# Performance work log

Measured on AMD Instinct MI355X. Metric: run time of the kernel, lower is better.

## Reference

```python
import jax, jax.numpy as jnp
import numpy as np

N_HEADS = 16
D_IN = 1024
D_K = 64          # per-head
D_V_HEAD = 1024 // N_HEADS  # 64 per-head


def setup_inputs() -> dict:
    key = jax.random.key(0)
    k1, k2, k3, k4, k5 = jax.random.split(key, 5)
    B, LQ, LK = 2, 2048, 2048
    s = 1.0 / np.sqrt(D_IN)
    return {
        "input_q": jax.random.normal(k1, (B, LQ, D_IN), dtype=jnp.float32),
        "input_k": jax.random.normal(k2, (B, LK, D_IN), dtype=jnp.float32),
        # nn.Linear weights stored as [out, in]; we use [in, out] for x @ W
        "wq": jax.random.uniform(k3, (D_IN, D_K * N_HEADS), jnp.float32, -s, s),
        "wk": jax.random.uniform(k4, (D_IN, D_K * N_HEADS), jnp.float32, -s, s),
        "wv": jax.random.uniform(k5, (D_IN, D_V_HEAD * N_HEADS), jnp.float32, -s, s),
    }


def reference(input_q, input_k, wq, wk, wv):
    B, LQ, _ = input_q.shape
    _, LK, _ = input_k.shape
    # project and split heads: [B, H, L, d]
    q = (input_q @ wq).reshape(B, LQ, N_HEADS, D_K).transpose(0, 2, 1, 3)
    k = (input_k @ wk).reshape(B, LK, N_HEADS, D_K).transpose(0, 2, 1, 3)
    v = (input_k @ wv).reshape(B, LK, N_HEADS, D_V_HEAD).transpose(0, 2, 1, 3)
    attn = jnp.einsum("bhqd,bhkd->bhqk", q, k) / jnp.sqrt(jnp.float32(D_K))
    attn = jax.nn.softmax(attn, axis=-1)
    out = jnp.einsum("bhqk,bhkd->bhqd", attn, v)
    return out.transpose(0, 2, 1, 3).reshape(B, LQ, D_V_HEAD * N_HEADS)
```

## Files before the change

kernel.cpp:

```cpp
#include <hip/hip_runtime.h>

#define DIN 1024
#define LSEQ 2048

typedef _Float16 f16;
typedef _Float16 half8 __attribute__((ext_vector_type(8)));
typedef float floatx4 __attribute__((ext_vector_type(4)));

__device__ __forceinline__ void async_ld16(const void* g, void* l) {
  __builtin_amdgcn_global_load_lds(
      (const __attribute__((address_space(1))) void*)g,
      (__attribute__((address_space(3))) void*)l, 16, 0, 0);
}

__device__ __forceinline__ float fast_exp2(float x) {
#if __has_builtin(__builtin_amdgcn_exp2f)
  return __builtin_amdgcn_exp2f(x);
#else
  return exp2f(x);
#endif
}

__device__ __forceinline__ unsigned int pack2_f16(float a, float b) {
#if __has_builtin(__builtin_amdgcn_cvt_pkrtz)
  typedef __fp16 fp16x2 __attribute__((ext_vector_type(2)));
  fp16x2 h = __builtin_amdgcn_cvt_pkrtz(a, b);
  return __builtin_bit_cast(unsigned int, h);
#else
  union { f16 h[2]; unsigned int u; } pk;
  pk.h[0] = (f16)a; pk.h[1] = (f16)b;
  return pk.u;
#endif
}

__global__ void __launch_bounds__(256) kprep(const float* __restrict__ xq,
                                             const float* __restrict__ xk,
                                             const float* __restrict__ wq,
                                             const float* __restrict__ wk,
                                             const float* __restrict__ wv,
                                             f16* __restrict__ wqt,
                                             f16* __restrict__ wkt,
                                             f16* __restrict__ wvt,
                                             f16* __restrict__ xqh,
                                             f16* __restrict__ xkh) {
  int z = blockIdx.z;
  int tid = threadIdx.x;
  if (z < 3) {
    __shared__ float t[32][33];
    const float* src = z == 0 ? wq : (z == 1 ? wk : wv);
    f16* dst = z == 0 ? wqt : (z == 1 ? wkt : wvt);
    int k0 = blockIdx.x * 32, n0 = blockIdx.y * 32;
    int tx = tid & 31, ty = tid >> 5;
#pragma unroll
    for (int r = 0; r < 4; ++r)
      t[ty + r * 8][tx] = src[(k0 + ty + r * 8) * DIN + n0 + tx];
    __syncthreads();
#pragma unroll
    for (int r = 0; r < 4; ++r)
      dst[(n0 + ty + r * 8) * DIN + k0 + tx] = (f16)t[tx][ty + r * 8];
  } else {
    const float4* src = (const float4*)(z == 4 ? xk : xq);
    uint2* dst = (uint2*)(z == 4 ? xkh : xqh);
    int bx = blockIdx.y * 32 + blockIdx.x;
    int i = bx * 256 + tid;
#pragma unroll
    for (int it = 0; it < 4; ++it, i += 262144) {
      float4 v = src[i];
      union { unsigned int u[2]; uint2 w; } pk;
      pk.u[0] = pack2_f16(v.x, v.y);
      pk.u[1] = pack2_f16(v.z, v.w);
      dst[i] = pk.w;
    }
  }
}

template <int AMODE>
__global__ void __launch_bounds__(256) kproj(const float* __restrict__ xq,
                                             const float* __restrict__ xk,
                                             const f16* __restrict__ xqh,
                                             const f16* __restrict__ xkh,
                                             const f16* __restrict__ wqt,
                                             const f16* __restrict__ wkt,
                                             const f16* __restrict__ wvt,
                                             f16* __restrict__ qb,
                                             f16* __restrict__ kb,
                                             f16* __restrict__ vtb) {
  __shared__ __align__(16) char smem[34816];
  char* As = smem;
  char* Bs = smem + 16384;
  const float* X;
  const f16* Xh;
  const f16* W;
  int z = blockIdx.z;
  if (z == 0) { X = xq; Xh = xqh; W = wqt; }
  else if (z == 1) { X = xk; Xh = xkh; W = wkt; }
  else { X = xk; Xh = xkh; W = wvt; }
  float oscale = (z == 0) ? 0.18033688011112042f : 1.0f;
  int m0 = blockIdx.y * 128, n0 = blockIdx.x * 128;
  int tid = threadIdx.x, lane = tid & 63, wid = tid >> 6;
  int wm = wid >> 1, wn = wid & 1;
  int c15 = lane & 15, g = lane >> 4;
  int l8 = lane >> 3, l7 = lane & 7;
  int kk = 8 * (l7 ^ l8);
  int swz = (c15 & 7) << 4;
  floatx4 acc[4][4] = {};

  for (int kt = 0; kt < 16; ++kt) {
    int k0 = kt * 64;
    if constexpr (AMODE == 1) {
#pragma unroll
      for (int cc = 0; cc < 4; ++cc) {
        int c = wid * 4 + cc;
        async_ld16(&Xh[(m0 + c * 8 + l8) * DIN + k0 + kk], As + c * 1024);
        async_ld16(&W[(n0 + c * 8 + l8) * DIN + k0 + kk], Bs + c * 1024);
      }
    } else {
#pragma unroll
      for (int cc = 0; cc < 4; ++cc) {
        int c = wid * 4 + cc;
        async_ld16(&W[(n0 + c * 8 + l8) * DIN + k0 + kk], Bs + c * 1024);
      }
      int q = tid & 15;
#pragma unroll
      for (int p = 0; p < 8; ++p) {
        int row = p * 16 + (tid >> 4);
        const float4 v = *(const float4*)&X[(m0 + row) * DIN + k0 + q * 4];
        union { unsigned int u[2]; uint2 v2; } pk;
        pk.u[0] = pack2_f16(v.x, v.y);
        pk.u[1] = pack2_f16(v.z, v.w);
        *(uint2*)(As + row * 128 + ((q * 8) ^ ((row & 7) << 4))) = pk.v2;
      }
    }
    __syncthreads();
#pragma unroll
    for (int ks = 0; ks < 2; ++ks) {
      int koff = (ks * 64 + g * 16) ^ swz;
      half8 af[4], bf[4];
#pragma unroll
      for (int i = 0; i < 4; ++i)
        af[i] = *(const half8*)(As + (wm * 64 + i * 16 + c15) * 128 + koff);
#pragma unroll
      for (int j = 0; j < 4; ++j)
        bf[j] = *(const half8*)(Bs + (wn * 64 + j * 16 + c15) * 128 + koff);
#pragma unroll
      for (int i = 0; i < 4; ++i)
#pragma unroll
        for (int j = 0; j < 4; ++j)
          acc[i][j] = __builtin_amdgcn_mfma_f32_16x16x32_f16(af[i], bf[j], acc[i][j], 0, 0, 0);
    }
    __syncthreads();
  }

  if (z != 2) {
    f16* dst = (z == 0) ? qb : kb;
#pragma unroll
    for (int i = 0; i < 4; ++i) {
      int mrow = m0 + wm * 64 + i * 16 + 4 * g;
#pragma unroll
      for (int j = 0; j < 4; ++j) {
        int n = n0 + wn * 64 + j * 16 + c15;
        int h = n >> 6, d = n & 63;
#pragma unroll
        for (int r = 0; r < 4; ++r) {
          int m = mrow + r;
          int b = m >> 11, lrow = m & 2047;
          dst[(((b << 4) + h) * 2048 + lrow) * 64 + d] = (f16)(acc[i][j][r] * oscale);
        }
      }
    }
  } else {
#pragma unroll
    for (int i = 0; i < 4; ++i) {
      int mb = (wm * 64 + i * 16 + 4 * g) * 2;
#pragma unroll
      for (int j = 0; j < 4; ++j) {
        int nl = wn * 64 + j * 16 + c15;
        union { unsigned int u[2]; uint2 v; } pk;
        pk.u[0] = pack2_f16(acc[i][j][0], acc[i][j][1]);
        pk.u[1] = pack2_f16(acc[i][j][2], acc[i][j][3]);
        *(uint2*)(smem + nl * 272 + mb) = pk.v;
      }
    }
    __syncthreads();
    int rowp = tid >> 1, halfp = tid & 1;
    int n = n0 + rowp, h = n >> 6, d = n & 63;
    int b = m0 >> 11, lbase = m0 & 2047;
    f16* dstp = vtb + (((size_t)b * 16 + h) * 64 + d) * 2048 + lbase + halfp * 64;
    const char* srcl = smem + rowp * 272 + halfp * 128;
#pragma unroll
    for (int u = 0; u < 8; ++u)
      *(uint4*)(dstp + u * 8) = *(const uint4*)(srcl + u * 16);
  }
}

__global__ void __launch_bounds__(256, 2) kattn(const f16* __restrict__ qb,
                                                const f16* __restrict__ kbuf,
                                                const f16* __restrict__ vt,
                                                float* __restrict__ out) {
  __shared__ __align__(16) char smem[81920];
  char* Qs = smem + 65536;
  float* Ot = (float*)smem;
  float* lsb = (float*)(smem + 34816);

  int id = blockIdx.x;
  int wi = id >> 3;
  int bh = ((id & 7) << 2) | (wi >> 4);
  int q0 = (wi & 15) << 7;

  int tid = threadIdx.x, lane = tid & 63, w = tid >> 6;
  int c15 = lane & 15, g = lane >> 4;
  int l8 = lane >> 3, l7 = lane & 7;
  int kk = 8 * (l7 ^ l8);
  int swz = (c15 & 7) << 4;

  const f16* kbase = kbuf + (size_t)bh * 2048 * 64;
  const f16* vbase = vt + (size_t)bh * 64 * 2048;

  auto stageK = [&](int b, int kv0) {
#pragma unroll
    for (int cc = 0; cc < 4; ++cc) {
      int c = w * 4 + cc;
      async_ld16(&kbase[(kv0 + c * 8 + l8) * 64 + kk],
                 smem + b * 16384 + c * 1024);
    }
  };
  auto stageV = [&](int b, int kv0) {
#pragma unroll
    for (int cc = 0; cc < 4; ++cc) {
      int c = w * 4 + cc;
      int hb = c >> 3;
      int dv = (c & 7) * 8 + l8;
      async_ld16(&vbase[(size_t)dv * 2048 + kv0 + 64 * hb + kk],
                 smem + 32768 + b * 16384 + c * 1024);
    }
  };

#pragma unroll
  for (int cc = 0; cc < 4; ++cc) {
    int c = w * 4 + cc;
    async_ld16(&qb[((size_t)bh * 2048 + q0 + c * 8 + l8) * 64 + kk],
               Qs + c * 1024);
  }
  stageK(0, 0);
  stageV(0, 0);
  __syncthreads();
  half8 qf[2][2];
#pragma unroll
  for (int s = 0; s < 2; ++s)
#pragma unroll
    for (int ks = 0; ks < 2; ++ks)
      qf[s][ks] = *(const half8*)(Qs + (w * 32 + s * 16 + c15) * 128 +
                                  ((ks * 64 + g * 16) ^ swz));
  __syncthreads();

  float ls0 = 0.f, ls1 = 0.f;
  floatx4 oacc[2][4] = {};
  char* Pw0 = smem + 65536 + (w * 2 + 0) * 2048 + c15 * 128;
  char* Pw1 = smem + 65536 + (w * 2 + 1) * 2048 + c15 * 128;
  int psw = swz;

  for (int t = 0; t < 16; ++t) {
    int buf = t & 1;
    if (t < 15) {
      stageK(buf ^ 1, (t + 1) * 128);
      stageV(buf ^ 1, (t + 1) * 128);
    }

    floatx4 st[2][8] = {};
    __builtin_amdgcn_s_setprio(1);
#pragma unroll
    for (int hb = 0; hb < 2; ++hb) {
      const char* Ks = smem + buf * 16384 + hb * 8192;
#pragma unroll
      for (int ks = 0; ks < 2; ++ks) {
        int koff = (ks * 64 + g * 16) ^ swz;
#pragma unroll
        for (int i = 0; i < 4; ++i) {
          half8 kf = *(const half8*)(Ks + (i * 16 + c15) * 128 + koff);
          st[0][hb * 4 + i] = __builtin_amdgcn_mfma_f32_16x16x32_f16(
              kf, qf[0][ks], st[0][hb * 4 + i], 0, 0, 0);
          st[1][hb * 4 + i] = __builtin_amdgcn_mfma_f32_16x16x32_f16(
              kf, qf[1][ks], st[1][hb * 4 + i], 0, 0, 0);
        }
      }
    }
    __builtin_amdgcn_s_setprio(0);

    unsigned int pu0[16], pu1[16];
    {
      float ps0 = 0.f, ps1 = 0.f;
#pragma unroll
      for (int x = 0; x < 16; ++x) {
        float p0 = fast_exp2(st[0][x >> 1][(x & 1) * 2]);
        float p1 = fast_exp2(st[0][x >> 1][(x & 1) * 2 + 1]);
        ps0 += p0;
        ps1 += p1;
        pu0[x] = pack2_f16(p0, p1);
      }
      ls0 += ps0 + ps1;
    }
    {
      float ps0 = 0.f, ps1 = 0.f;
#pragma unroll
      for (int x = 0; x < 16; ++x) {
        float p0 = fast_exp2(st[1][x >> 1][(x & 1) * 2]);
        float p1 = fast_exp2(st[1][x >> 1][(x & 1) * 2 + 1]);
        ps0 += p0;
        ps1 += p1;
        pu1[x] = pack2_f16(p0, p1);
      }
      ls1 += ps0 + ps1;
    }

    __builtin_amdgcn_s_setprio(1);
#pragma unroll
    for (int hb = 0; hb < 2; ++hb) {
#pragma unroll
      for (int ii = 0; ii < 4; ++ii) {
        union { unsigned int u[2]; uint2 v; } pk;
        pk.u[0] = pu0[hb * 8 + 2 * ii];
        pk.u[1] = pu0[hb * 8 + 2 * ii + 1];
        *(uint2*)(Pw0 + ((32 * ii + 8 * g) ^ psw)) = pk.v;
        pk.u[0] = pu1[hb * 8 + 2 * ii];
        pk.u[1] = pu1[hb * 8 + 2 * ii + 1];
        *(uint2*)(Pw1 + ((32 * ii + 8 * g) ^ psw)) = pk.v;
      }
      const char* Vs = smem + 32768 + buf * 16384 + hb * 8192;
#pragma unroll
      for (int kb = 0; kb < 2; ++kb) {
        half8 pf0 = *(const half8*)(Pw0 + ((kb * 64 + 16 * g) ^ psw));
        half8 pf1 = *(const half8*)(Pw1 + ((kb * 64 + 16 * g) ^ psw));
        int koff = (kb * 64 + g * 16) ^ swz;
#pragma unroll
        for (int df = 0; df < 4; ++df) {
          half8 vf = *(const half8*)(Vs + (df * 16 + c15) * 128 + koff);
          oacc[0][df] = __builtin_amdgcn_mfma_f32_16x16x32_f16(vf, pf0, oacc[0][df], 0, 0, 0);
          oacc[1][df] = __builtin_amdgcn_mfma_f32_16x16x32_f16(vf, pf1, oacc[1][df], 0, 0, 0);
        }
      }
    }
    __builtin_amdgcn_s_setprio(0);
    __syncthreads();
  }

  ls0 += __shfl_xor(ls0, 16, 64);
  ls0 += __shfl_xor(ls0, 32, 64);
  ls1 += __shfl_xor(ls1, 16, 64);
  ls1 += __shfl_xor(ls1, 32, 64);
  if (g == 0) {
    lsb[w * 32 + c15] = ls0;
    lsb[w * 32 + 16 + c15] = ls1;
  }

#pragma unroll
  for (int s = 0; s < 2; ++s)
#pragma unroll
    for (int df = 0; df < 4; ++df)
      *(floatx4*)&Ot[(w * 32 + s * 16 + c15) * 68 + df * 16 + 4 * g] =
          oacc[s][df];
  __syncthreads();

  int b = bh >> 4, h = bh & 15;
  int row = tid >> 1, seg = tid & 1;
  float inv = 1.f / lsb[row];
  float* dstp = &out[((size_t)b * 2048 + q0 + row) * 1024 + h * 64 + seg * 32];
  const float* srcl = &Ot[row * 68 + seg * 32];
#pragma unroll
  for (int u = 0; u < 8; ++u) {
    floatx4 v = *(const floatx4*)(srcl + u * 4) * inv;
    *(floatx4*)(dstp + u * 4) = v;
  }
}

extern "C" void kernel_launch(void* const* d_in, const int* in_sizes, int n_in,
                              void* d_out, int out_size, void* d_ws, size_t ws_size,
                              hipStream_t stream) {
  const float* xq = (const float*)d_in[0];
  const float* xk = (const float*)d_in[1];
  const float* wq = (const float*)d_in[2];
  const float* wk = (const float*)d_in[3];
  const float* wv = (const float*)d_in[4];
  char* ws = (char*)d_ws;
  f16* wqt = (f16*)(ws + (0ull << 20));
  f16* wkt = (f16*)(ws + (2ull << 20));
  f16* wvt = (f16*)(ws + (4ull << 20));

  bool fit = ws_size >= (46ull << 20);
  f16 *xqh, *xkh, *qbuf, *kbuf, *vtb;
  if (fit) {
    xqh  = (f16*)(ws + (6ull << 20));
    xkh  = (f16*)(ws + (14ull << 20));
    qbuf = (f16*)(ws + (22ull << 20));
    kbuf = (f16*)(ws + (30ull << 20));
    vtb  = (f16*)(ws + (38ull << 20));
  } else {
    xqh = xkh = nullptr;
    qbuf = (f16*)(ws + (6ull << 20));
    kbuf = (f16*)(ws + (14ull << 20));
    vtb  = (f16*)(ws + (22ull << 20));
  }

  kprep<<<dim3(32, 32, fit ? 5 : 3), 256, 0, stream>>>(xq, xk, wq, wk, wv,
                                                       wqt, wkt, wvt, xqh, xkh);
  if (fit) {
    kproj<1><<<dim3(8, 32, 3), 256, 0, stream>>>(xq, xk, xqh, xkh, wqt, wkt,
                                                 wvt, qbuf, kbuf, vtb);
  } else {
    kproj<0><<<dim3(8, 32, 3), 256, 0, stream>>>(xq, xk, xqh, xkh, wqt, wkt,
                                                 wvt, qbuf, kbuf, vtb);
  }
  kattn<<<512, 256, 0, stream>>>(qbuf, kbuf, vtb, (float*)d_out);
}
```

Measured before the change: 103.8 us.

## Software-pipeline QK^T of next tile with softmax/PV of current tile

Restructures the attention main loop into a two-stage software pipeline. The QK^T MMAs for the next KV tile are issued before the exp/pack/PV work of the current tile, using two score register sets and separate K/V buffer staging. The aim is to overlap matrix-core work with the exp and LDS traffic that currently serialise within each iteration. It doubles the score accumulator registers, which risks spills or lower occupancy under launch_bounds(256,2).

```diff
diff --git a/kernel.cpp b/kernel.cpp
--- a/kernel.cpp
+++ b/kernel.cpp
@@ -198,6 +198,10 @@
                                                 const f16* __restrict__ vt,
                                                 float* __restrict__ out) {
   __shared__ __align__(16) char smem[81920];
+  char* kb0 = smem;
+  char* kb1 = smem + 16384;
+  char* vb0 = smem + 32768;
+  char* vb1 = smem + 49152;
   char* Qs = smem + 65536;
   float* Ot = (float*)smem;
   float* lsb = (float*)(smem + 34816);
@@ -216,22 +220,21 @@
   const f16* kbase = kbuf + (size_t)bh * 2048 * 64;
   const f16* vbase = vt + (size_t)bh * 64 * 2048;
 
-  auto stageK = [&](int b, int kv0) {
+  auto stageK = [&](char* dstb, int kv0) {
 #pragma unroll
     for (int cc = 0; cc < 4; ++cc) {
       int c = w * 4 + cc;
-      async_ld16(&kbase[(kv0 + c * 8 + l8) * 64 + kk],
-                 smem + b * 16384 + c * 1024);
+      async_ld16(&kbase[(kv0 + c * 8 + l8) * 64 + kk], dstb + c * 1024);
     }
   };
-  auto stageV = [&](int b, int kv0) {
+  auto stageV = [&](char* dstb, int kv0) {
 #pragma unroll
     for (int cc = 0; cc < 4; ++cc) {
       int c = w * 4 + cc;
       int hb = c >> 3;
       int dv = (c & 7) * 8 + l8;
       async_ld16(&vbase[(size_t)dv * 2048 + kv0 + 64 * hb + kk],
-                 smem + 32768 + b * 16384 + c * 1024);
+                 dstb + c * 1024);
     }
   };
 
@@ -241,8 +244,8 @@
     async_ld16(&qb[((size_t)bh * 2048 + q0 + c * 8 + l8) * 64 + kk],
                Qs + c * 1024);
   }
-  stageK(0, 0);
-  stageV(0, 0);
+  stageK(kb0, 0);
+  stageV(vb0, 0);
   __syncthreads();
   half8 qf[2][2];
 #pragma unroll
@@ -259,89 +262,107 @@
   char* Pw1 = smem + 65536 + (w * 2 + 1) * 2048 + c15 * 128;
   int psw = swz;
 
-  for (int t = 0; t < 16; ++t) {
-    int buf = t & 1;
-    if (t < 15) {
-      stageK(buf ^ 1, (t + 1) * 128);
-      stageV(buf ^ 1, (t + 1) * 128);
-    }
-
-    floatx4 st[2][8] = {};
-    __builtin_amdgcn_s_setprio(1);
-#pragma unroll
-    for (int hb = 0; hb < 2; ++hb) {
-      const char* Ks = smem + buf * 16384 + hb * 8192;
-#pragma unroll
-      for (int ks = 0; ks < 2; ++ks) {
-        int koff = (ks * 64 + g * 16) ^ swz;
-#pragma unroll
-        for (int i = 0; i < 4; ++i) {
-          half8 kf = *(const half8*)(Ks + (i * 16 + c15) * 128 + koff);
-          st[0][hb * 4 + i] = __builtin_amdgcn_mfma_f32_16x16x32_f16(
-              kf, qf[0][ks], st[0][hb * 4 + i], 0, 0, 0);
-          st[1][hb * 4 + i] = __builtin_amdgcn_mfma_f32_16x16x32_f16(
-              kf, qf[1][ks], st[1][hb * 4 + i], 0, 0, 0);
-        }
-      }
-    }
-    __builtin_amdgcn_s_setprio(0);
-
-    unsigned int pu0[16], pu1[16];
-    {
-      float ps0 = 0.f, ps1 = 0.f;
-#pragma unroll
-      for (int x = 0; x < 16; ++x) {
-        float p0 = fast_exp2(st[0][x >> 1][(x & 1) * 2]);
-        float p1 = fast_exp2(st[0][x >> 1][(x & 1) * 2 + 1]);
-        ps0 += p0;
-        ps1 += p1;
-        pu0[x] = pack2_f16(p0, p1);
-      }
-      ls0 += ps0 + ps1;
-    }
-    {
-      float ps0 = 0.f, ps1 = 0.f;
-#pragma unroll
-      for (int x = 0; x < 16; ++x) {
-        float p0 = fast_exp2(st[1][x >> 1][(x & 1) * 2]);
-        float p1 = fast_exp2(st[1][x >> 1][(x & 1) * 2 + 1]);
-        ps0 += p0;
-        ps1 += p1;
-        pu1[x] = pack2_f16(p0, p1);
-      }
-      ls1 += ps0 + ps1;
-    }
-
-    __builtin_amdgcn_s_setprio(1);
-#pragma unroll
-    for (int hb = 0; hb < 2; ++hb) {
-#pragma unroll
-      for (int ii = 0; ii < 4; ++ii) {
-        union { unsigned int u[2]; uint2 v; } pk;
-        pk.u[0] = pu0[hb * 8 + 2 * ii];
-        pk.u[1] = pu0[hb * 8 + 2 * ii + 1];
-        *(uint2*)(Pw0 + ((32 * ii + 8 * g) ^ psw)) = pk.v;
-        pk.u[0] = pu1[hb * 8 + 2 * ii];
-        pk.u[1] = pu1[hb * 8 + 2 * ii + 1];
-        *(uint2*)(Pw1 + ((32 * ii + 8 * g) ^ psw)) = pk.v;
-      }
-      const char* Vs = smem + 32768 + buf * 16384 + hb * 8192;
-#pragma unroll
-      for (int kb = 0; kb < 2; ++kb) {
-        half8 pf0 = *(const half8*)(Pw0 + ((kb * 64 + 16 * g) ^ psw));
-        half8 pf1 = *(const half8*)(Pw1 + ((kb * 64 + 16 * g) ^ psw));
-        int koff = (kb * 64 + g * 16) ^ swz;
-#pragma unroll
-        for (int df = 0; df < 4; ++df) {
-          half8 vf = *(const half8*)(Vs + (df * 16 + c15) * 128 + koff);
-          oacc[0][df] = __builtin_amdgcn_mfma_f32_16x16x32_f16(vf, pf0, oacc[0][df], 0, 0, 0);
-          oacc[1][df] = __builtin_amdgcn_mfma_f32_16x16x32_f16(vf, pf1, oacc[1][df], 0, 0, 0);
-        }
-      }
-    }
-    __builtin_amdgcn_s_setprio(0);
-    __syncthreads();
-  }
+#define QK_TILE(ST, KB)                                                      \
+  {                                                                          \
+    __builtin_amdgcn_s_setprio(1);                                           \
+    _Pragma("unroll") for (int hb = 0; hb < 2; ++hb) {                       \
+      const char* Ks = (KB) + hb * 8192;                                     \
+      _Pragma("unroll") for (int ks = 0; ks < 2; ++ks) {                     \
+        int koff = (ks * 64 + g * 16) ^ swz;                                 \
+        _Pragma("unroll") for (int i = 0; i < 4; ++i) {                      \
+          half8 kf = *(const half8*)(Ks + (i * 16 + c15) * 128 + koff);      \
+          ST[0][hb * 4 + i] = __builtin_amdgcn_mfma_f32_16x16x32_f16(        \
+              kf, qf[0][ks], ST[0][hb * 4 + i], 0, 0, 0);                    \
+          ST[1][hb * 4 + i] = __builtin_amdgcn_mfma_f32_16x16x32_f16(        \
+              kf, qf[1][ks], ST[1][hb * 4 + i], 0, 0, 0);                    \
+        }                                                                    \
+      }                                                                      \
+    }                                                                        \
+    __builtin_amdgcn_s_setprio(0);                                           \
+  }
+
+#define ZERO_ST(ST)                                                          \
+  _Pragma("unroll") for (int z1 = 0; z1 < 2; ++z1)                           \
+      _Pragma("unroll") for (int z2 = 0; z2 < 8; ++z2) ST[z1][z2] = {};
+
+#define SMPV_TILE(ST, VB)                                                    \
+  {                                                                          \
+    unsigned int pu0[16], pu1[16];                                           \
+    {                                                                        \
+      float ps0 = 0.f, ps1 = 0.f;                                            \
+      _Pragma("unroll") for (int x = 0; x < 16; ++x) {                       \
+        float p0 = fast_exp2(ST[0][x >> 1][(x & 1) * 2]);                    \
+        float p1 = fast_exp2(ST[0][x >> 1][(x & 1) * 2 + 1]);                \
+        ps0 += p0;                                                           \
+        ps1 += p1;                                                           \
+        pu0[x] = pack2_f16(p0, p1);                                          \
+      }                                                                      \
+      ls0 += ps0 + ps1;                                                      \
+    }                                                                        \
+    {                                                                        \
+      float ps0 = 0.f, ps1 = 0.f;                                            \
+      _Pragma("unroll") for (int x = 0; x < 16; ++x) {                       \
+        float p0 = fast_exp2(ST[1][x >> 1][(x & 1) * 2]);                    \
+        float p1 = fast_exp2(ST[1][x >> 1][(x & 1) * 2 + 1]);                \
+        ps0 += p0;                                                           \
+        ps1 += p1;                                                           \
+        pu1[x] = pack2_f16(p0, p1);                                          \
+      }                                                                      \
+      ls1 += ps0 + ps1;                                                      \
+    }                                                                        \
+    __builtin_amdgcn_s_setprio(1);                                           \
+    _Pragma("unroll") for (int hb = 0; hb < 2; ++hb) {                       \
+      _Pragma("unroll") for (int ii = 0; ii < 4; ++ii) {                     \
+        union { unsigned int u[2]; uint2 v; } pk;                            \
+        pk.u[0] = pu0[hb * 8 + 2 * ii];                                      \
+        pk.u[1] = pu0[hb * 8 + 2 * ii + 1];                                  \
+        *(uint2*)(Pw0 + ((32 * ii + 8 * g) ^ psw)) = pk.v;                   \
+        pk.u[0] = pu1[hb * 8 + 2 * ii];                                      \
+        pk.u[1] = pu1[hb * 8 + 2 * ii + 1];                                  \
+        *(uint2*)(Pw1 + ((32 * ii + 8 * g) ^ psw)) = pk.v;                   \
+      }                                                                      \
+      const char* Vs = (VB) + hb * 8192;                                     \
+      _Pragma("unroll") for (int kb = 0; kb < 2; ++kb) {                     \
+        half8 pf0 = *(const half8*)(Pw0 + ((kb * 64 + 16 * g) ^ psw));       \
+        half8 pf1 = *(const half8*)(Pw1 + ((kb * 64 + 16 * g) ^ psw));       \
+        int koff = (kb * 64 + g * 16) ^ swz;                                 \
+        _Pragma("unroll") for (int df = 0; df < 4; ++df) {                   \
+          half8 vf = *(const half8*)(Vs + (df * 16 + c15) * 128 + koff);     \
+          oacc[0][df] = __builtin_amdgcn_mfma_f32_16x16x32_f16(              \
+              vf, pf0, oacc[0][df], 0, 0, 0);                                \
+          oacc[1][df] = __builtin_amdgcn_mfma_f32_16x16x32_f16(              \
+              vf, pf1, oacc[1][df], 0, 0, 0);                                \
+        }                                                                    \
+      }                                                                      \
+    }                                                                        \
+    __builtin_amdgcn_s_setprio(0);                                           \
+  }
+
+  stageK(kb1, 128);
+  floatx4 stA[2][8], stB[2][8];
+  ZERO_ST(stA);
+  QK_TILE(stA, kb0);
+  __syncthreads();
+
+  for (int p = 0; p < 8; ++p) {
+    if (p < 7) stageK(kb0, (2 * p + 2) * 128);
+    stageV(vb1, (2 * p + 1) * 128);
+    ZERO_ST(stB);
+    QK_TILE(stB, kb1);
+    SMPV_TILE(stA, vb0);
+    __syncthreads();
+    if (p < 7) {
+      stageK(kb1, (2 * p + 3) * 128);
+      stageV(vb0, (2 * p + 2) * 128);
+      ZERO_ST(stA);
+      QK_TILE(stA, kb0);
+    }
+    SMPV_TILE(stB, vb1);
+    __syncthreads();
+  }
+#undef QK_TILE
+#undef ZERO_ST
+#undef SMPV_TILE
 
   ls0 += __shfl_xor(ls0, 16, 64);
   ls0 += __shfl_xor(ls0, 32, 64);
```

Result: slower. 134.9 us (+30.0%).
